# Optimization experiments

Measured on AMD Instinct MI355X. Metric: run time of the kernel, lower is better.

## Reference

```python
import jax, jax.numpy as jnp
import numpy as np

# ---- static config ----
B, N, C, HF, WF = 2, 256, 256, 64, 64
PATCH = 512
ROI = 15
MARGIN = (ROI - 1) // 2
HID = 256
HEADS = 8
DEPTH = 3
FFN = 1024
NQ = 16
LN_EPS = 1e-5


def setup_inputs() -> dict:
    key = jax.random.key(0)
    ks = jax.random.split(key, 16)
    p = lambda i, shape: (0.02 * jax.random.normal(ks[i], shape, jnp.float32))
    inp = {
        "image_embeddings": jax.random.normal(ks[0], (B, C, HF, WF), jnp.float32),
        "keypoints": jax.random.uniform(ks[1], (B, N, 2), jnp.float32, 0.0, float(PATCH)),
        "keypoints_valid_mask": jax.random.randint(ks[2], (B, N), 0, 2) == 1,
        "proj_w": p(3, (HID, C)), "proj_b": jnp.zeros((HID,), jnp.float32),
        "query_embed": p(4, (NQ, HID)),
        "self_qkv_w": p(5, (DEPTH, 3 * HID, HID)), "self_qkv_b": jnp.zeros((DEPTH, 3 * HID), jnp.float32),
        "self_out_w": p(6, (DEPTH, HID, HID)), "self_out_b": jnp.zeros((DEPTH, HID), jnp.float32),
        "cross_qkv_w": p(7, (DEPTH, 3 * HID, HID)), "cross_qkv_b": jnp.zeros((DEPTH, 3 * HID), jnp.float32),
        "cross_out_w": p(8, (DEPTH, HID, HID)), "cross_out_b": jnp.zeros((DEPTH, HID), jnp.float32),
        "ffn1_w": p(9, (DEPTH, FFN, HID)), "ffn1_b": jnp.zeros((DEPTH, FFN), jnp.float32),
        "ffn2_w": p(10, (DEPTH, HID, FFN)), "ffn2_b": jnp.zeros((DEPTH, HID), jnp.float32),
        "ln1_w": jnp.ones((DEPTH, HID), jnp.float32), "ln1_b": jnp.zeros((DEPTH, HID), jnp.float32),
        "ln2_w": jnp.ones((DEPTH, HID), jnp.float32), "ln2_b": jnp.zeros((DEPTH, HID), jnp.float32),
        "ln3_w": jnp.ones((DEPTH, HID), jnp.float32), "ln3_b": jnp.zeros((DEPTH, HID), jnp.float32),
        "out_w": p(11, (4, HID)), "out_b": jnp.zeros((4,), jnp.float32),
    }
    return inp


def _layer_norm(x, w, b):
    mu = x.mean(-1, keepdims=True)
    var = ((x - mu) ** 2).mean(-1, keepdims=True)
    return (x - mu) * jax.lax.rsqrt(var + LN_EPS) * w + b


def _mha(q_in, kv_in, Wqkv, bqkv, Wo, bo, pad=None):
    # PyTorch nn.MultiheadAttention math (batch_first). pad: [B, S_kv] True=masked.
    Dh = HID // HEADS
    Wq, Wk, Wv = jnp.split(Wqkv, 3, axis=0)
    bq, bk, bv = jnp.split(bqkv, 3, axis=0)
    Bsz = q_in.shape[0]
    q = (q_in @ Wq.T + bq).reshape(Bsz, -1, HEADS, Dh)
    k = (kv_in @ Wk.T + bk).reshape(Bsz, -1, HEADS, Dh)
    v = (kv_in @ Wv.T + bv).reshape(Bsz, -1, HEADS, Dh)
    s = jnp.einsum('bqhd,bkhd->bhqk', q, k) * (Dh ** -0.5)
    if pad is not None:
        s = jnp.where(pad[:, None, None, :], -jnp.inf, s)
    a = jax.nn.softmax(s, axis=-1)
    o = jnp.einsum('bhqk,bkhd->bqhd', a, v).reshape(Bsz, -1, HID)
    return o @ Wo.T + bo


def _roi_sample(img, keypoints):
    # _get_valid_grid + F.grid_sample(bilinear, align_corners=False, zeros padding)
    rc = jnp.round(keypoints)                               # [B,N,2] (r,c), round-half-even like Python round
    off = jnp.arange(-MARGIN, MARGIN + 1, dtype=img.dtype)  # [ROI]
    gy = rc[:, :, 0][..., None, None] + off[:, None]        # [B,N,ROI,ROI] rows
    gx = rc[:, :, 1][..., None, None] + off[None, :]        # [B,N,ROI,ROI] cols
    gxn = gx / (PATCH - 1) * 2.0 - 1.0
    gyn = gy / (PATCH - 1) * 2.0 - 1.0
    invalid = (gxn < -1) | (gyn < -1) | (gxn > 1) | (gyn > 1)  # [B,N,ROI,ROI]
    gxn = jnp.where(invalid, 0.0, gxn)
    gyn = jnp.where(invalid, 0.0, gyn)
    # unnormalize onto the feature map (align_corners=False)
    x = ((gxn + 1.0) * WF - 1.0) * 0.5
    y = ((gyn + 1.0) * HF - 1.0) * 0.5
    x = x.reshape(B, -1)  # [B, P], P = N*ROI*ROI
    y = y.reshape(B, -1)
    x0f = jnp.floor(x); y0f = jnp.floor(y)
    wx = x - x0f; wy = y - y0f
    x0 = x0f.astype(jnp.int32); y0 = y0f.astype(jnp.int32)
    bidx = jnp.arange(B)[:, None]

    def tap(yi, xi, w):
        ok = (yi >= 0) & (yi < HF) & (xi >= 0) & (xi < WF)
        yc = jnp.clip(yi, 0, HF - 1)
        xc = jnp.clip(xi, 0, WF - 1)
        v = img[bidx, :, yc, xc]                 # [B,P,C] gather
        return v * (w * ok)[..., None]

    out = (tap(y0, x0, (1 - wy) * (1 - wx)) + tap(y0, x0 + 1, (1 - wy) * wx)
           + tap(y0 + 1, x0, wy * (1 - wx)) + tap(y0 + 1, x0 + 1, wy * wx))
    feat = out.reshape(B, N, ROI * ROI, C)
    feat = jnp.where(invalid.reshape(B, N, ROI * ROI)[..., None], 0.0, feat)
    return feat  # [B, N, HW, C]


def reference(image_embeddings, keypoints, keypoints_valid_mask, proj_w, proj_b,
              query_embed, self_qkv_w, self_qkv_b, self_out_w, self_out_b,
              cross_qkv_w, cross_qkv_b, cross_out_w, cross_out_b,
              ffn1_w, ffn1_b, ffn2_w, ffn2_b,
              ln1_w, ln1_b, ln2_w, ln2_b, ln3_w, ln3_b, out_w, out_b):
    feat = _roi_sample(image_embeddings, keypoints)                 # [B,N,HW,C]
    mem = jnp.einsum('bnpc,oc->bnpo', feat, proj_w) + proj_b        # 1x1 conv proj
    mem = mem.reshape(B * N, ROI * ROI, HID)
    pad = jnp.broadcast_to(~keypoints_valid_mask.reshape(-1, 1), (B * N, ROI * ROI))
    pad = pad.at[:, 0].set(False)                                    # token 0 always attendable
    tgt = jnp.broadcast_to(query_embed[None], (B * N, NQ, HID))
    for l in range(DEPTH):  # post-norm TransformerDecoderLayer, relu, eval (no dropout)
        sa = _mha(tgt, tgt, self_qkv_w[l], self_qkv_b[l], self_out_w[l], self_out_b[l])
        tgt = _layer_norm(tgt + sa, ln1_w[l], ln1_b[l])
        ca = _mha(tgt, mem, cross_qkv_w[l], cross_qkv_b[l], cross_out_w[l], cross_out_b[l], pad)
        tgt = _layer_norm(tgt + ca, ln2_w[l], ln2_b[l])
        ff = jax.nn.relu(tgt @ ffn1_w[l].T + ffn1_b[l]) @ ffn2_w[l].T + ffn2_b[l]
        tgt = _layer_norm(tgt + ff, ln3_w[l], ln3_b[l])
    out = tgt @ out_w.T + out_b                                      # [B*N, NQ, 4]
    return out.reshape(B, N, NQ, 4)
```

## Files before the change

kernel.cpp:

```cpp
#include <hip/hip_runtime.h>
#include <hip/hip_fp16.h>

#define LB __launch_bounds__(256)

typedef unsigned short u16;
typedef unsigned int   u32;
typedef __attribute__((ext_vector_type(8))) short bf16x8;
typedef __attribute__((ext_vector_type(4))) float f32x4;
typedef __attribute__((ext_vector_type(8))) u16  u16x8;

__device__ __forceinline__ u16 f2b(float f) {
    u32 u = __float_as_uint(f);
    u32 r = (u + 0x7fffu + ((u >> 16) & 1u)) >> 16;
    return (u16)r;
}
__device__ __forceinline__ float b2f(u16 h) {
    return __uint_as_float((u32)h << 16);
}

#define QSCALE 0.17677669529663687f


__global__ LB void k_wconv(const float* __restrict__ s0, const float* __restrict__ s1,
                           const float* __restrict__ s2, const float* __restrict__ s3,
                           const float* __restrict__ s4, const float* __restrict__ s5,
                           const float* __restrict__ s6, u16* __restrict__ dst,
                           const unsigned char* __restrict__ m, int* __restrict__ valid,
                           const float* __restrict__ pb,
                           const float* __restrict__ cqkv_b,
                           float* __restrict__ ckv)
{
    if (blockIdx.x >= 14336) {
        const int pblk = blockIdx.x - 14336;
        if (pblk == 0) {
            __shared__ int flag;
            if (threadIdx.x == 0) flag = 0;
            __syncthreads();
            int loc = 0;
            for (int off = threadIdx.x; off < 512; off += 256)
                if ((off & 3) != 0 && m[off] != 0) loc = 1;
            if (loc) atomicOr(&flag, 1);
            __syncthreads();
            const bool bytelay = (flag != 0);
            for (int s = threadIdx.x; s < 512; s += 256)
                valid[s] = bytelay ? (int)(m[s] != 0) : (int)(((const int*)m)[s] != 0);
        } else {
            const int l = pblk - 1;
            const float* Wv = s3 + (size_t)l * 196608 + 131072;
            const float* vb = cqkv_b + (size_t)l * 768 + 512;
            const int o = threadIdx.x;
            float c = 0.f;
            for (int cc = 0; cc < 256; cc += 4) {
                const float4 p4 = *(const float4*)(pb + cc);
                const float4 v4 = *(const float4*)(Wv + (size_t)o * 256 + cc);
                c += p4.x * v4.x + p4.y * v4.y + p4.z * v4.z + p4.w * v4.w;
            }
            ckv[l * 512 + o]       = cqkv_b[(size_t)l * 768 + o];
            ckv[l * 512 + 256 + o] = c + vb[o];
        }
        return;
    }
    const int e = blockIdx.x * 256 + threadIdx.x;
    if (e >= 3670016) return;
    float v;
    int i = e;
    if (i < 65536) v = s0[i];
    else if ((i -= 65536) < 589824) v = s1[i];
    else if ((i -= 589824) < 196608) v = s2[i];
    else if ((i -= 196608) < 589824) v = s3[i];
    else if ((i -= 589824) < 196608) v = s4[i];
    else if ((i -= 196608) < 786432) v = s5[i];
    else if ((i -= 786432) < 786432) v = s6[i];
    else if ((i -= 786432) < 393216) {
        const int l = i / 131072;
        const int r = (i - l * 131072) >> 8;
        const int c = i & 255;
        v = s3[(size_t)l * 196608 + (size_t)(256 + r) * 256 + c];
    } else {
        i -= 393216;
        v = s0[(i & 255) * 256 + (i >> 8)];
    }
    dst[e] = f2b(v);
}

__global__ LB void k_transpose(const float* __restrict__ img, u16* __restrict__ imgTb)
{
    __shared__ float tile[64][65];
    const int b  = blockIdx.z;
    const int c0 = blockIdx.y * 64;
    const int p0 = blockIdx.x * 64;
    const int t  = threadIdx.x;
    const int tr = t >> 6, tc = t & 63;
#pragma unroll
    for (int p = 0; p < 16; ++p) {
        const int i = p * 4 + tr;
        tile[i][tc] = img[((size_t)(b * 256 + c0 + i)) * 4096 + p0 + tc];
    }
    __syncthreads();
#pragma unroll
    for (int p = 0; p < 16; ++p) {
        const int jj = p * 4 + tr;
        imgTb[((size_t)(b * 4096 + p0 + jj)) * 256 + c0 + tc] = f2b(tile[tc][jj]);
    }
}

template<int BM>
__global__ LB void gemm_mfma(const u16* __restrict__ A, const u16* __restrict__ W,
                             const float* __restrict__ bias,
                             float* __restrict__ Cf, u16* __restrict__ Cb,
                             int M, int N, int K, int relu)
{
    constexpr int BN = 128;
    __shared__ u16 lds[2][(BM + BN) * 64];
    const int t = threadIdx.x;
    const int wid = t >> 6, lane = t & 63;
    const int bm = blockIdx.y * BM, bn = blockIdx.x * BN;
    const int KT = K >> 6;

    auto stage = [&](int buf, int kt) {
        const int k0 = kt * 64;
        const int rr = t >> 3;
        const int u  = t & 7;
#pragma unroll
        for (int q = 0; q < BM / 32; ++q) {
            const int r = q * 32 + rr;
            const u16* src = A + (size_t)(bm + r) * K + k0 + ((u ^ (r & 7)) << 3);
            __builtin_amdgcn_global_load_lds(
                (const __attribute__((address_space(1))) void*)src,
                (__attribute__((address_space(3))) void*)&lds[buf][q * 2048 + wid * 512],
                16, 0, 0);
        }
#pragma unroll
        for (int q = 0; q < 4; ++q) {
            const int r = q * 32 + rr;
            const u16* src = W + (size_t)(bn + r) * K + k0 + ((u ^ (r & 7)) << 3);
            __builtin_amdgcn_global_load_lds(
                (const __attribute__((address_space(1))) void*)src,
                (__attribute__((address_space(3))) void*)&lds[buf][BM * 64 + q * 2048 + wid * 512],
                16, 0, 0);
        }
    };

    const int wr = wid >> 1, wc = wid & 1;
    constexpr int MR = BM / 32;
    f32x4 acc[MR][4];
    const f32x4 z = {0.f, 0.f, 0.f, 0.f};
#pragma unroll
    for (int mi = 0; mi < MR; ++mi)
#pragma unroll
        for (int ni = 0; ni < 4; ++ni) acc[mi][ni] = z;

    const int r16 = lane & 15, kg = lane >> 4;

    stage(0, 0);
    int cur = 0;
    for (int kt = 0; kt < KT; ++kt) {
        asm volatile("s_waitcnt vmcnt(0)" ::: "memory");
        __syncthreads();
        if (kt + 1 < KT) stage(cur ^ 1, kt + 1);
        const u16* pA = lds[cur];
        const u16* pB = lds[cur] + BM * 64;
#pragma unroll
        for (int kk = 0; kk < 2; ++kk) {
            const int s = kk * 4 + kg;
            bf16x8 afr[MR], bfr[4];
#pragma unroll
            for (int mi = 0; mi < MR; ++mi) {
                const int r = wr * (BM / 2) + mi * 16 + r16;
                afr[mi] = *(const bf16x8*)(pA + r * 64 + ((s ^ (r & 7)) << 3));
            }
#pragma unroll
            for (int ni = 0; ni < 4; ++ni) {
                const int c = wc * 64 + ni * 16 + r16;
                bfr[ni] = *(const bf16x8*)(pB + c * 64 + ((s ^ (c & 7)) << 3));
            }
#pragma unroll
            for (int mi = 0; mi < MR; ++mi)
#pragma unroll
                for (int ni = 0; ni < 4; ++ni)
                    acc[mi][ni] = __builtin_amdgcn_mfma_f32_16x16x32_bf16(
                        afr[mi], bfr[ni], acc[mi][ni], 0, 0, 0);
        }
        cur ^= 1;
    }

#pragma unroll
    for (int mi = 0; mi < MR; ++mi) {
#pragma unroll
        for (int ni = 0; ni < 4; ++ni) {
            const int col = bn + wc * 64 + ni * 16 + r16;
            const float bs = bias ? bias[col] : 0.0f;
#pragma unroll
            for (int rg = 0; rg < 4; ++rg) {
                const int row = bm + wr * (BM / 2) + mi * 16 + kg * 4 + rg;
                float v = acc[mi][ni][rg] + bs;
                if (relu) v = fmaxf(v, 0.0f);
                if (Cf) Cf[(size_t)row * N + col] = v;
                if (Cb) Cb[(size_t)row * N + col] = f2b(v);
            }
        }
    }
}

__global__ LB void gemm_ln(const u16* __restrict__ A, const u16* __restrict__ W,
                           const float* __restrict__ bias,
                           float* __restrict__ tgt, u16* __restrict__ tgtb,
                           const float* __restrict__ lnw, const float* __restrict__ lnb,
                           int K,
                           const float* __restrict__ ow, const float* __restrict__ ob,
                           float* __restrict__ outp)
{
    __shared__ u16 lA[32 * 64];
    __shared__ u16 lB[256 * 64];
    __shared__ float psum[2][32];
    __shared__ float psq[2][32];
    __shared__ float hsum[2][32][4];
    const int t = threadIdx.x;
    const int wid = t >> 6, lane = t & 63;
    const int r16 = lane & 15, kg = lane >> 4;
    const int wr = wid >> 1, wc = wid & 1;
    const int bm = blockIdx.x * 32;
    const int KT = K >> 6;

    f32x4 acc[8];
    const f32x4 z = {0.f, 0.f, 0.f, 0.f};
#pragma unroll
    for (int ni = 0; ni < 8; ++ni) acc[ni] = z;

    for (int kt = 0; kt < KT; ++kt) {
        const int k0 = kt * 64;
        const int rr = t >> 3;
        const int u  = t & 7;
        {
            const int r = rr;
            const u16* src = A + (size_t)(bm + r) * K + k0 + ((u ^ (r & 7)) << 3);
            __builtin_amdgcn_global_load_lds(
                (const __attribute__((address_space(1))) void*)src,
                (__attribute__((address_space(3))) void*)&lA[wid * 512],
                16, 0, 0);
        }
#pragma unroll
        for (int q = 0; q < 8; ++q) {
            const int r = q * 32 + rr;
            const u16* src = W + (size_t)r * K + k0 + ((u ^ (r & 7)) << 3);
            __builtin_amdgcn_global_load_lds(
                (const __attribute__((address_space(1))) void*)src,
                (__attribute__((address_space(3))) void*)&lB[q * 2048 + wid * 512],
                16, 0, 0);
        }
        asm volatile("s_waitcnt vmcnt(0)" ::: "memory");
        __syncthreads();
#pragma unroll
        for (int kk = 0; kk < 2; ++kk) {
            const int s = kk * 4 + kg;
            const int ra = wr * 16 + r16;
            const bf16x8 afr = *(const bf16x8*)(lA + ra * 64 + ((s ^ (ra & 7)) << 3));
#pragma unroll
            for (int ni = 0; ni < 8; ++ni) {
                const int c = wc * 128 + ni * 16 + r16;
                const bf16x8 bfr = *(const bf16x8*)(lB + c * 64 + ((s ^ (c & 7)) << 3));
                acc[ni] = __builtin_amdgcn_mfma_f32_16x16x32_bf16(afr, bfr, acc[ni], 0, 0, 0);
            }
        }
        __syncthreads();
    }

    float xv[4][8];
    float bcol[8], wcol[8], bncol[8];
#pragma unroll
    for (int ni = 0; ni < 8; ++ni) {
        const int c = wc * 128 + ni * 16 + r16;
        bcol[ni]  = bias[c];
        wcol[ni]  = lnw[c];
        bncol[ni] = lnb[c];
    }
#pragma unroll
    for (int rg = 0; rg < 4; ++rg) {
        const int row = bm + wr * 16 + kg * 4 + rg;
#pragma unroll
        for (int ni = 0; ni < 8; ++ni) {
            const int c = wc * 128 + ni * 16 + r16;
            xv[rg][ni] = tgt[(size_t)row * 256 + c] + acc[ni][rg] + bcol[ni];
        }
    }
#pragma unroll
    for (int rg = 0; rg < 4; ++rg) {
        float s = 0.f;
#pragma unroll
        for (int ni = 0; ni < 8; ++ni) s += xv[rg][ni];
#pragma unroll
        for (int m = 1; m < 16; m <<= 1) s += __shfl_xor(s, m);
        if (r16 == 0) psum[wc][wr * 16 + kg * 4 + rg] = s;
    }
    __syncthreads();
    float mu[4];
#pragma unroll
    for (int rg = 0; rg < 4; ++rg) {
        const int rl = wr * 16 + kg * 4 + rg;
        mu[rg] = (psum[0][rl] + psum[1][rl]) * (1.0f / 256.0f);
    }
#pragma unroll
    for (int rg = 0; rg < 4; ++rg) {
        float q = 0.f;
#pragma unroll
        for (int ni = 0; ni < 8; ++ni) {
            const float d = xv[rg][ni] - mu[rg];
            q += d * d;
        }
#pragma unroll
        for (int m = 1; m < 16; m <<= 1) q += __shfl_xor(q, m);
        if (r16 == 0) psq[wc][wr * 16 + kg * 4 + rg] = q;
    }
    __syncthreads();
    float onorm[4][8];
#pragma unroll
    for (int rg = 0; rg < 4; ++rg) {
        const int rl = wr * 16 + kg * 4 + rg;
        const int row = bm + rl;
        const float var = (psq[0][rl] + psq[1][rl]) * (1.0f / 256.0f);
        const float inv = 1.0f / sqrtf(var + 1e-5f);
#pragma unroll
        for (int ni = 0; ni < 8; ++ni) {
            const int c = wc * 128 + ni * 16 + r16;
            const float o = (xv[rg][ni] - mu[rg]) * inv * wcol[ni] + bncol[ni];
            onorm[rg][ni] = o;
            tgt[(size_t)row * 256 + c]  = o;
            tgtb[(size_t)row * 256 + c] = f2b(o);
        }
    }

    if (outp) {
#pragma unroll
        for (int j = 0; j < 4; ++j) {
            float wj[8];
#pragma unroll
            for (int ni = 0; ni < 8; ++ni)
                wj[ni] = ow[j * 256 + wc * 128 + ni * 16 + r16];
#pragma unroll
            for (int rg = 0; rg < 4; ++rg) {
                float p = 0.f;
#pragma unroll
                for (int ni = 0; ni < 8; ++ni) p += onorm[rg][ni] * wj[ni];
#pragma unroll
                for (int m = 1; m < 16; m <<= 1) p += __shfl_xor(p, m);
                if (r16 == 0) hsum[wc][wr * 16 + kg * 4 + rg][j] = p;
            }
        }
        __syncthreads();
        if (t < 128) {
            const int row = t >> 2, j = t & 3;
            outp[(size_t)(bm + row) * 4 + j] =
                hsum[0][row][j] + hsum[1][row][j] + ob[j];
        }
    }
}

__global__ LB void k_init_tgt(float* __restrict__ tgt, u16* __restrict__ tgtb,
                              const float* __restrict__ qe)
{
    const int e = blockIdx.x * 256 + threadIdx.x;
    const int c = e & 255;
    const int row = e >> 8;
    const int i = row & 15;
    const float v = qe[(i << 8) | c];
    tgt[e] = v;
    tgtb[e] = f2b(v);
}

__global__ LB void k_self_attn(const u16* __restrict__ QKV, u16* __restrict__ O)
{
    __shared__ __align__(16) u16 arena[4][1536];
    const int t = threadIdx.x;
    const int lane = t & 63, wid = t >> 6;
    const int r16 = lane & 15, kg = lane >> 4;
    const int blk = blockIdx.x;
    const int s = blk >> 1;
    const int h = (blk & 1) * 4 + wid;

    u16* p_lds = &arena[wid][0];
    u16* vT    = &arena[wid][512];

    const bf16x8 qfr = *(const bf16x8*)(QKV + (size_t)(s * 16 + r16) * 768 + h * 32 + kg * 8);
    const bf16x8 kfr = *(const bf16x8*)(QKV + (size_t)(s * 16 + r16) * 768 + 256 + h * 32 + kg * 8);
    f32x4 sv = {0.f, 0.f, 0.f, 0.f};
    sv = __builtin_amdgcn_mfma_f32_16x16x32_bf16(qfr, kfr, sv, 0, 0, 0);

    float ev[4], rowsum[4];
#pragma unroll
    for (int rg = 0; rg < 4; ++rg) ev[rg] = sv[rg] * QSCALE;
#pragma unroll
    for (int rg = 0; rg < 4; ++rg) {
        float mx = ev[rg];
#pragma unroll
        for (int m = 1; m < 16; m <<= 1) mx = fmaxf(mx, __shfl_xor(mx, m));
        ev[rg] = __expf(ev[rg] - mx);
        float ps = ev[rg];
#pragma unroll
        for (int m = 1; m < 16; m <<= 1) ps += __shfl_xor(ps, m);
        rowsum[rg] = ps;
    }

#pragma unroll
    for (int rg = 0; rg < 4; ++rg)
        p_lds[(kg * 4 + rg) * 32 + r16] = f2b(ev[rg]);
    {
        const int zq = lane & 15, zc = 16 + (lane >> 4) * 4;
#pragma unroll
        for (int j = 0; j < 4; ++j) p_lds[zq * 32 + zc + j] = 0;
    }
    {
        const int key = lane >> 2, ch8 = (lane & 3) * 8;
        const u16x8 v = *(const u16x8*)(QKV + (size_t)(s * 16 + key) * 768 + 512 + h * 32 + ch8);
#pragma unroll
        for (int j = 0; j < 8; ++j)
            vT[(ch8 + j) * 32 + key] = ((const u16*)&v)[j];
        const int zc0 = lane >> 1, zk0 = 16 + (lane & 1) * 8;
#pragma unroll
        for (int j = 0; j < 8; ++j) vT[zc0 * 32 + zk0 + j] = 0;
    }

#pragma unroll
    for (int ct = 0; ct < 2; ++ct) {
        const bf16x8 pa = *(const bf16x8*)(p_lds + r16 * 32 + kg * 8);
        const bf16x8 vb = *(const bf16x8*)(vT + (ct * 16 + r16) * 32 + kg * 8);
        f32x4 ao = {0.f, 0.f, 0.f, 0.f};
        ao = __builtin_amdgcn_mfma_f32_16x16x32_bf16(pa, vb, ao, 0, 0, 0);
#pragma unroll
        for (int rg = 0; rg < 4; ++rg) {
            const int q = kg * 4 + rg;
            O[(size_t)(s * 16 + q) * 256 + h * 32 + ct * 16 + r16] = f2b(ao[rg] / rowsum[rg]);
        }
    }
}

__global__ LB void k_cross_attn(const u16* __restrict__ tgtb,
                                const u16* __restrict__ wQ,
                                const u16* __restrict__ KV, int kvs,
                                const float* __restrict__ ckv,
                                const int* __restrict__ valid,
                                const float* __restrict__ kps,
                                u16* __restrict__ O)
{
    __shared__ __align__(16) char arena[64832];
    u16* Wm  = (u16*)arena;
    u16* WmT = (u16*)(arena + 14400);

    const int t = threadIdx.x;
    const int lane = t & 63, wid = t >> 6;
    const int r16 = lane & 15, kg = lane >> 4;
    const int s = blockIdx.x;
    const int b = s >> 8, n = s & 255;

    u16* buf = (u16*)(arena + 22848 + wid * 10496);
    u16* p_b = (u16*)(arena + 22848 + wid * 10496 + 2048);
    u16* QP  = p_b;

    for (int e = t; e < 16208; e += 256) ((u32*)arena)[e] = 0;
    __syncthreads();

    const float kpy = kps[(b * 256 + n) * 2 + 0];
    const float kpx = kps[(b * 256 + n) * 2 + 1];
    const float gx0 = rintf(kpx) - 7.0f;
    const float gy0 = rintf(kpy) - 7.0f;
    const float gxn0 = gx0 / 511.0f * 2.0f - 1.0f;
    const float gyn0 = gy0 / 511.0f * 2.0f - 1.0f;
    const float xb = ((gxn0 + 1.f) * 64.f - 1.f) * 0.5f;
    const float yb = ((gyn0 + 1.f) * 64.f - 1.f) * 0.5f;
    const int x0b = (int)floorf(xb);
    const int y0b = (int)floorf(yb);

    if (t < 225) {
        const int iy = t / 15, ix = t - iy * 15;
        const float gy = rintf(kpy) + (float)(iy - 7);
        const float gx = rintf(kpx) + (float)(ix - 7);
        const float gxn = gx / 511.0f * 2.0f - 1.0f;
        const float gyn = gy / 511.0f * 2.0f - 1.0f;
        const bool inval = (gxn < -1.f) || (gyn < -1.f) || (gxn > 1.f) || (gyn > 1.f);
        const float x = ((gxn + 1.f) * 64.f - 1.f) * 0.5f;
        const float y = ((gyn + 1.f) * 64.f - 1.f) * 0.5f;
        const float x0f = floorf(x), y0f = floorf(y);
        const float wx = x - x0f, wy = y - y0f;
        const int x0 = (int)x0f, y0 = (int)y0f;
#pragma unroll
        for (int tt = 0; tt < 4; ++tt) {
            const int dy = tt >> 1, dx = tt & 1;
            const int yi = y0 + dy, xi = x0 + dx;
            const bool ok = (yi >= 0) && (yi < 64) && (xi >= 0) && (xi < 64) && !inval;
            const float w = (dy ? wy : 1.f - wy) * (dx ? wx : 1.f - wx);
            if (ok) {
                const int cell = (yi - y0b) * 4 + (xi - x0b);
                const u16 wb = f2b(w);
                Wm[t * 32 + ((((cell >> 3) ^ (t & 3)) << 3) | (cell & 7))] = wb;
                WmT[cell * 264 + t] = wb;
            }
        }
    }

    const int cell = lane >> 2, ch8 = (lane & 3) * 8;
    const int cy = cell >> 2, cx = cell & 3;
    const int py = min(max(y0b + cy, 0), 63);
    const int px = min(max(x0b + cx, 0), 63);
    const bool vld = valid[s] != 0;

    for (int hh = 0; hh < 2; ++hh) {
        const int h = hh * 4 + wid;
        const size_t texidx = (size_t)(b * 4096 + py * 64 + px) * kvs + h * 32 + ch8;

#pragma unroll
        for (int ct = 0; ct < 2; ++ct) {
            f32x4 aq = {0.f, 0.f, 0.f, 0.f};
#pragma unroll
            for (int ks = 0; ks < 8; ++ks) {
                const bf16x8 ta = *(const bf16x8*)(tgtb + (size_t)(s * 16 + r16) * 256 + ks * 32 + kg * 8);
                const bf16x8 wb = *(const bf16x8*)(wQ + (size_t)(h * 32 + ct * 16 + r16) * 256 + ks * 32 + kg * 8);
                aq = __builtin_amdgcn_mfma_f32_16x16x32_bf16(ta, wb, aq, 0, 0, 0);
            }
            const float bq = ckv[h * 32 + ct * 16 + r16];
#pragma unroll
            for (int rg = 0; rg < 4; ++rg)
                QP[(kg * 4 + rg) * 40 + ct * 16 + r16] = f2b(aq[rg] + bq);
        }
        *(u16x8*)(buf + cell * 32 + ch8) = *(const u16x8*)(KV + texidx);

        if (hh == 0) __syncthreads();

        {
            const bf16x8 qfr = *(const bf16x8*)(QP + r16 * 40 + kg * 8);
            const bf16x8 tfr = *(const bf16x8*)(buf + r16 * 32 + kg * 8);
            f32x4 aq = {0.f, 0.f, 0.f, 0.f};
            aq = __builtin_amdgcn_mfma_f32_16x16x32_bf16(qfr, tfr, aq, 0, 0, 0);
#pragma unroll
            for (int rg = 0; rg < 4; ++rg)
                QP[(kg * 4 + rg) * 40 + r16] = f2b(aq[rg]);
        }

        float ev[4][15];
        {
            const bf16x8 afr = *(const bf16x8*)(QP + r16 * 40 + kg * 8);
#pragma unroll
            for (int tile = 0; tile < 15; ++tile) {
                const int p = tile * 16 + r16;
                const int rc = p < 225 ? p : 224;
                const bf16x8 bfr = *(const bf16x8*)(Wm + rc * 32 + ((kg ^ (rc & 3)) << 3));
                f32x4 acc = {0.f, 0.f, 0.f, 0.f};
                acc = __builtin_amdgcn_mfma_f32_16x16x32_bf16(afr, bfr, acc, 0, 0, 0);
#pragma unroll
                for (int rg = 0; rg < 4; ++rg) {
                    float sv = acc[rg] * QSCALE;
                    if (p > 224) sv = -1e30f;
                    if (!vld && p > 0) sv = -1e30f;
                    ev[rg][tile] = sv;
                }
            }
        }
        float rowsumv[4];
#pragma unroll
        for (int rg = 0; rg < 4; ++rg) {
            float mx = -1e30f;
#pragma unroll
            for (int k = 0; k < 15; ++k) mx = fmaxf(mx, ev[rg][k]);
#pragma unroll
            for (int m = 1; m < 16; m <<= 1) mx = fmaxf(mx, __shfl_xor(mx, m));
            float ps = 0.f;
#pragma unroll
            for (int k = 0; k < 15; ++k) {
                ev[rg][k] = __expf(ev[rg][k] - mx);
                ps += ev[rg][k];
            }
#pragma unroll
            for (int m = 1; m < 16; m <<= 1) ps += __shfl_xor(ps, m);
            rowsumv[rg] = ps;
        }

#pragma unroll
        for (int rg = 0; rg < 4; ++rg)
#pragma unroll
            for (int k = 0; k < 15; ++k) {
                const int p = k * 16 + r16;
                if (p < 225) p_b[(kg * 4 + rg) * 264 + p] = f2b(ev[rg][k]);
            }
        for (int e = lane; e < 496; e += 64) {
            const int row = e / 31;
            p_b[row * 264 + 225 + (e - row * 31)] = 0;
        }

        {
            const u16x8 v = *(const u16x8*)(KV + texidx + 256);
#pragma unroll
            for (int j = 0; j < 8; ++j)
                buf[(ch8 + j) * 32 + cell] = ((const u16*)&v)[j];
            const int zr = lane & 15, zc0 = 16 + (lane >> 4) * 4;
#pragma unroll
            for (int j = 0; j < 4; ++j) buf[zr * 32 + zc0 + j] = 0;
        }

        f32x4 pw = {0.f, 0.f, 0.f, 0.f};
#pragma unroll
        for (int ks = 0; ks < 8; ++ks) {
            const bf16x8 pa = *(const bf16x8*)(p_b + r16 * 264 + ks * 32 + kg * 8);
            const bf16x8 wb = *(const bf16x8*)(WmT + r16 * 264 + ks * 32 + kg * 8);
            pw = __builtin_amdgcn_mfma_f32_16x16x32_bf16(pa, wb, pw, 0, 0, 0);
        }

#pragma unroll
        for (int rg = 0; rg < 4; ++rg)
            QP[(kg * 4 + rg) * 40 + r16] = f2b(pw[rg]);
        {
            const int zq = lane & 15, zc0 = 16 + (lane >> 4) * 4;
#pragma unroll
            for (int j = 0; j < 4; ++j) QP[zq * 40 + zc0 + j] = 0;
        }

#pragma unroll
        for (int ct = 0; ct < 2; ++ct) {
            const bf16x8 pa = *(const bf16x8*)(QP + r16 * 40 + kg * 8);
            const bf16x8 vb = *(const bf16x8*)(buf + (ct * 16 + r16) * 32 + kg * 8);
            f32x4 ao = {0.f, 0.f, 0.f, 0.f};
            ao = __builtin_amdgcn_mfma_f32_16x16x32_bf16(pa, vb, ao, 0, 0, 0);
#pragma unroll
            for (int rg = 0; rg < 4; ++rg) {
                const int q = kg * 4 + rg;
                const int ch = h * 32 + ct * 16 + r16;
                const float val = ao[rg] / rowsumv[rg] + ckv[256 + ch];
                O[(size_t)(s * 16 + q) * 256 + ch] = f2b(val);
            }
        }
    }
}

extern "C" void kernel_launch(void* const* d_in, const int* in_sizes, int n_in,
                              void* d_out, int out_size, void* d_ws, size_t ws_size,
                              hipStream_t stream)
{
    const float* img          = (const float*)d_in[0];
    const float* kps          = (const float*)d_in[1];
    const unsigned char* vmsk = (const unsigned char*)d_in[2];
    const float* proj_w       = (const float*)d_in[3];
    const float* proj_b       = (const float*)d_in[4];
    const float* query_embed  = (const float*)d_in[5];
    const float* self_qkv_w   = (const float*)d_in[6];
    const float* self_qkv_b   = (const float*)d_in[7];
    const float* self_out_w   = (const float*)d_in[8];
    const float* self_out_b   = (const float*)d_in[9];
    const float* cross_qkv_w  = (const float*)d_in[10];
    const float* cross_qkv_b  = (const float*)d_in[11];
    const float* cross_out_w  = (const float*)d_in[12];
    const float* cross_out_b  = (const float*)d_in[13];
    const float* ffn1_w       = (const float*)d_in[14];
    const float* ffn1_b       = (const float*)d_in[15];
    const float* ffn2_w       = (const float*)d_in[16];
    const float* ffn2_b       = (const float*)d_in[17];
    const float* ln1_w        = (const float*)d_in[18];
    const float* ln1_b        = (const float*)d_in[19];
    const float* ln2_w        = (const float*)d_in[20];
    const float* ln2_b        = (const float*)d_in[21];
    const float* ln3_w        = (const float*)d_in[22];
    const float* ln3_b        = (const float*)d_in[23];
    const float* out_w        = (const float*)d_in[24];
    const float* out_b        = (const float*)d_in[25];
    float* out = (float*)d_out;

    char* W8 = (char*)d_ws;
    size_t off = 0;
    auto alloc = [&](size_t bytes) { void* p = W8 + off; off += (bytes + 255) & ~(size_t)255; return p; };
    float* tgt   = (float*)alloc(2097152 * 4);
    u16* Sb16    = (u16*)alloc(6291456 * 2);
    float* ckv   = (float*)alloc(3 * 512 * 4);
    u16* imgTb   = (u16*)alloc(2097152 * 2);
    u16* KVb3    = (u16*)alloc(12582912 * 2);
    u16* tgtb    = (u16*)alloc(2097152 * 2);
    u16* Abuf    = (u16*)alloc(2097152 * 2);
    u16* Hbuf    = (u16*)alloc(8388608 * 2);
    u16* wAll    = (u16*)alloc(3670016 * 2);
    u16* WcombB  = (u16*)alloc(393216 * 2);
    int* valid   = (int*)alloc(512 * 4);

    u16* wProj  = wAll;
    u16* wSQKV  = wProj + 65536;
    u16* wSOut  = wSQKV + 589824;
    u16* wCQKV  = wSOut + 196608;
    u16* wCOut  = wCQKV + 589824;
    u16* wF1    = wCOut + 196608;
    u16* wF2    = wF1 + 786432;
    u16* wCKV3  = wF2 + 786432;
    u16* wProjT = wCKV3 + 393216;

    k_wconv<<<14340, 256, 0, stream>>>(proj_w, self_qkv_w, self_out_w, cross_qkv_w,
                                       cross_out_w, ffn1_w, ffn2_w, wAll,
                                       vmsk, valid, proj_b, cross_qkv_b, ckv);
    k_transpose<<<dim3(64, 4, 2), 256, 0, stream>>>(img, imgTb);
    gemm_mfma<64><<<dim3(2, 24), 256, 0, stream>>>(wCKV3, wProjT, nullptr,
                                                   nullptr, WcombB, 1536, 256, 256, 0);
    gemm_mfma<64><<<dim3(12, 128), 256, 0, stream>>>(imgTb, WcombB, nullptr,
                                                     nullptr, KVb3, 8192, 1536, 256, 0);
    k_init_tgt<<<8192, 256, 0, stream>>>(tgt, tgtb, query_embed);

    for (int l = 0; l < 3; ++l) {
        const int last = (l == 2);
        gemm_mfma<64><<<dim3(6, 128), 256, 0, stream>>>(tgtb, wSQKV + (size_t)l * 196608,
            self_qkv_b + (size_t)l * 768, nullptr, Sb16, 8192, 768, 256, 0);
        k_self_attn<<<1024, 256, 0, stream>>>(Sb16, Abuf);
        gemm_ln<<<256, 256, 0, stream>>>(Abuf, wSOut + (size_t)l * 65536,
            self_out_b + (size_t)l * 256, tgt, tgtb,
            ln1_w + (size_t)l * 256, ln1_b + (size_t)l * 256, 256,
            nullptr, nullptr, nullptr);

        k_cross_attn<<<512, 256, 0, stream>>>(tgtb, wCQKV + (size_t)l * 196608,
                                              KVb3 + (size_t)l * 512, 1536,
                                              ckv + (size_t)l * 512, valid, kps, Abuf);
        gemm_ln<<<256, 256, 0, stream>>>(Abuf, wCOut + (size_t)l * 65536,
            cross_out_b + (size_t)l * 256, tgt, tgtb,
            ln2_w + (size_t)l * 256, ln2_b + (size_t)l * 256, 256,
            nullptr, nullptr, nullptr);

        gemm_mfma<64><<<dim3(8, 128), 256, 0, stream>>>(tgtb, wF1 + (size_t)l * 262144,
            ffn1_b + (size_t)l * 1024, nullptr, Hbuf, 8192, 1024, 256, 1);
        gemm_ln<<<256, 256, 0, stream>>>(Hbuf, wF2 + (size_t)l * 262144,
            ffn2_b + (size_t)l * 256, tgt, tgtb,
            ln3_w + (size_t)l * 256, ln3_b + (size_t)l * 256, 1024,
            last ? out_w : nullptr, last ? out_b : nullptr, last ? out : nullptr);
    }
}
```

Baseline: 353.7 us.

## Fold image transpose into weight-convert kernel, halve self-attn grid, hoist tgt loads

The separate image transpose kernel is merged into the weight conversion launch as 512 extra blocks, which removes one kernel launch. The self-attention kernel now has each block loop over both head groups for one sequence, so its grid shrinks from 1024 to 512 blocks. In cross-attention, the tgt A-fragments are loaded into registers once, before the head loop, instead of being reloaded inside it. The cost is more register pressure, and the k_wconv blocks now all reserve shared memory for the tile, which may lower their occupancy.

```diff
diff --git a/kernel.cpp b/kernel.cpp
--- a/kernel.cpp
+++ b/kernel.cpp
@@ -28,8 +28,10 @@
                            const unsigned char* __restrict__ m, int* __restrict__ valid,
                            const float* __restrict__ pb,
                            const float* __restrict__ cqkv_b,
-                           float* __restrict__ ckv)
+                           float* __restrict__ ckv,
+                           const float* __restrict__ img, u16* __restrict__ imgTb)
 {
+    __shared__ float tile[64][65];
     if (blockIdx.x >= 14336) {
         const int pblk = blockIdx.x - 14336;
         if (pblk == 0) {
@@ -44,7 +46,7 @@
             const bool bytelay = (flag != 0);
             for (int s = threadIdx.x; s < 512; s += 256)
                 valid[s] = bytelay ? (int)(m[s] != 0) : (int)(((const int*)m)[s] != 0);
-        } else {
+        } else if (pblk < 4) {
             const int l = pblk - 1;
             const float* Wv = s3 + (size_t)l * 196608 + 131072;
             const float* vb = cqkv_b + (size_t)l * 768 + 512;
@@ -57,6 +59,25 @@
             }
             ckv[l * 512 + o]       = cqkv_b[(size_t)l * 768 + o];
             ckv[l * 512 + 256 + o] = c + vb[o];
+        } else {
+            const int idx = pblk - 4;
+            const int b  = idx >> 8;
+            const int rem = idx & 255;
+            const int c0 = (rem >> 6) * 64;
+            const int p0 = (rem & 63) * 64;
+            const int t  = threadIdx.x;
+            const int tr = t >> 6, tc = t & 63;
+#pragma unroll
+            for (int p = 0; p < 16; ++p) {
+                const int i = p * 4 + tr;
+                tile[i][tc] = img[((size_t)(b * 256 + c0 + i)) * 4096 + p0 + tc];
+            }
+            __syncthreads();
+#pragma unroll
+            for (int p = 0; p < 16; ++p) {
+                const int jj = p * 4 + tr;
+                imgTb[((size_t)(b * 4096 + p0 + jj)) * 256 + c0 + tc] = f2b(tile[tc][jj]);
+            }
         }
         return;
     }
@@ -83,27 +104,6 @@
     dst[e] = f2b(v);
 }
 
-__global__ LB void k_transpose(const float* __restrict__ img, u16* __restrict__ imgTb)
-{
-    __shared__ float tile[64][65];
-    const int b  = blockIdx.z;
-    const int c0 = blockIdx.y * 64;
-    const int p0 = blockIdx.x * 64;
-    const int t  = threadIdx.x;
-    const int tr = t >> 6, tc = t & 63;
-#pragma unroll
-    for (int p = 0; p < 16; ++p) {
-        const int i = p * 4 + tr;
-        tile[i][tc] = img[((size_t)(b * 256 + c0 + i)) * 4096 + p0 + tc];
-    }
-    __syncthreads();
-#pragma unroll
-    for (int p = 0; p < 16; ++p) {
-        const int jj = p * 4 + tr;
-        imgTb[((size_t)(b * 4096 + p0 + jj)) * 256 + c0 + tc] = f2b(tile[tc][jj]);
-    }
-}
-
 template<int BM>
 __global__ LB void gemm_mfma(const u16* __restrict__ A, const u16* __restrict__ W,
                              const float* __restrict__ bias,
@@ -373,62 +373,64 @@
     const int t = threadIdx.x;
     const int lane = t & 63, wid = t >> 6;
     const int r16 = lane & 15, kg = lane >> 4;
-    const int blk = blockIdx.x;
-    const int s = blk >> 1;
-    const int h = (blk & 1) * 4 + wid;
+    const int s = blockIdx.x;
 
     u16* p_lds = &arena[wid][0];
     u16* vT    = &arena[wid][512];
 
-    const bf16x8 qfr = *(const bf16x8*)(QKV + (size_t)(s * 16 + r16) * 768 + h * 32 + kg * 8);
-    const bf16x8 kfr = *(const bf16x8*)(QKV + (size_t)(s * 16 + r16) * 768 + 256 + h * 32 + kg * 8);
-    f32x4 sv = {0.f, 0.f, 0.f, 0.f};
-    sv = __builtin_amdgcn_mfma_f32_16x16x32_bf16(qfr, kfr, sv, 0, 0, 0);
-
-    float ev[4], rowsum[4];
-#pragma unroll
-    for (int rg = 0; rg < 4; ++rg) ev[rg] = sv[rg] * QSCALE;
-#pragma unroll
-    for (int rg = 0; rg < 4; ++rg) {
-        float mx = ev[rg];
-#pragma unroll
-        for (int m = 1; m < 16; m <<= 1) mx = fmaxf(mx, __shfl_xor(mx, m));
-        ev[rg] = __expf(ev[rg] - mx);
-        float ps = ev[rg];
-#pragma unroll
-        for (int m = 1; m < 16; m <<= 1) ps += __shfl_xor(ps, m);
-        rowsum[rg] = ps;
-    }
-
-#pragma unroll
-    for (int rg = 0; rg < 4; ++rg)
-        p_lds[(kg * 4 + rg) * 32 + r16] = f2b(ev[rg]);
-    {
-        const int zq = lane & 15, zc = 16 + (lane >> 4) * 4;
-#pragma unroll
-        for (int j = 0; j < 4; ++j) p_lds[zq * 32 + zc + j] = 0;
-    }
-    {
-        const int key = lane >> 2, ch8 = (lane & 3) * 8;
-        const u16x8 v = *(const u16x8*)(QKV + (size_t)(s * 16 + key) * 768 + 512 + h * 32 + ch8);
-#pragma unroll
-        for (int j = 0; j < 8; ++j)
-            vT[(ch8 + j) * 32 + key] = ((const u16*)&v)[j];
-        const int zc0 = lane >> 1, zk0 = 16 + (lane & 1) * 8;
-#pragma unroll
-        for (int j = 0; j < 8; ++j) vT[zc0 * 32 + zk0 + j] = 0;
-    }
-
-#pragma unroll
-    for (int ct = 0; ct < 2; ++ct) {
-        const bf16x8 pa = *(const bf16x8*)(p_lds + r16 * 32 + kg * 8);
-        const bf16x8 vb = *(const bf16x8*)(vT + (ct * 16 + r16) * 32 + kg * 8);
-        f32x4 ao = {0.f, 0.f, 0.f, 0.f};
-        ao = __builtin_amdgcn_mfma_f32_16x16x32_bf16(pa, vb, ao, 0, 0, 0);
+    for (int hh = 0; hh < 2; ++hh) {
+        const int h = hh * 4 + wid;
+
+        const bf16x8 qfr = *(const bf16x8*)(QKV + (size_t)(s * 16 + r16) * 768 + h * 32 + kg * 8);
+        const bf16x8 kfr = *(const bf16x8*)(QKV + (size_t)(s * 16 + r16) * 768 + 256 + h * 32 + kg * 8);
+        f32x4 sv = {0.f, 0.f, 0.f, 0.f};
+        sv = __builtin_amdgcn_mfma_f32_16x16x32_bf16(qfr, kfr, sv, 0, 0, 0);
+
+        float ev[4], rowsum[4];
+#pragma unroll
+        for (int rg = 0; rg < 4; ++rg) ev[rg] = sv[rg] * QSCALE;
 #pragma unroll
         for (int rg = 0; rg < 4; ++rg) {
-            const int q = kg * 4 + rg;
-            O[(size_t)(s * 16 + q) * 256 + h * 32 + ct * 16 + r16] = f2b(ao[rg] / rowsum[rg]);
+            float mx = ev[rg];
+#pragma unroll
+            for (int m = 1; m < 16; m <<= 1) mx = fmaxf(mx, __shfl_xor(mx, m));
+            ev[rg] = __expf(ev[rg] - mx);
+            float ps = ev[rg];
+#pragma unroll
+            for (int m = 1; m < 16; m <<= 1) ps += __shfl_xor(ps, m);
+            rowsum[rg] = ps;
+        }
+
+#pragma unroll
+        for (int rg = 0; rg < 4; ++rg)
+            p_lds[(kg * 4 + rg) * 32 + r16] = f2b(ev[rg]);
+        {
+            const int zq = lane & 15, zc = 16 + (lane >> 4) * 4;
+#pragma unroll
+            for (int j = 0; j < 4; ++j) p_lds[zq * 32 + zc + j] = 0;
+        }
+        {
+            const int key = lane >> 2, ch8 = (lane & 3) * 8;
+            const u16x8 v = *(const u16x8*)(QKV + (size_t)(s * 16 + key) * 768 + 512 + h * 32 + ch8);
+#pragma unroll
+            for (int j = 0; j < 8; ++j)
+                vT[(ch8 + j) * 32 + key] = ((const u16*)&v)[j];
+            const int zc0 = lane >> 1, zk0 = 16 + (lane & 1) * 8;
+#pragma unroll
+            for (int j = 0; j < 8; ++j) vT[zc0 * 32 + zk0 + j] = 0;
+        }
+
+#pragma unroll
+        for (int ct = 0; ct < 2; ++ct) {
+            const bf16x8 pa = *(const bf16x8*)(p_lds + r16 * 32 + kg * 8);
+            const bf16x8 vb = *(const bf16x8*)(vT + (ct * 16 + r16) * 32 + kg * 8);
+            f32x4 ao = {0.f, 0.f, 0.f, 0.f};
+            ao = __builtin_amdgcn_mfma_f32_16x16x32_bf16(pa, vb, ao, 0, 0, 0);
+#pragma unroll
+            for (int rg = 0; rg < 4; ++rg) {
+                const int q = kg * 4 + rg;
+                O[(size_t)(s * 16 + q) * 256 + h * 32 + ct * 16 + r16] = f2b(ao[rg] / rowsum[rg]);
+            }
         }
     }
 }
@@ -502,6 +504,11 @@
     const int px = min(max(x0b + cx, 0), 63);
     const bool vld = valid[s] != 0;
 
+    bf16x8 ta[8];
+#pragma unroll
+    for (int ks = 0; ks < 8; ++ks)
+        ta[ks] = *(const bf16x8*)(tgtb + (size_t)(s * 16 + r16) * 256 + ks * 32 + kg * 8);
+
     for (int hh = 0; hh < 2; ++hh) {
         const int h = hh * 4 + wid;
         const size_t texidx = (size_t)(b * 4096 + py * 64 + px) * kvs + h * 32 + ch8;
@@ -511,9 +518,8 @@
             f32x4 aq = {0.f, 0.f, 0.f, 0.f};
 #pragma unroll
             for (int ks = 0; ks < 8; ++ks) {
-                const bf16x8 ta = *(const bf16x8*)(tgtb + (size_t)(s * 16 + r16) * 256 + ks * 32 + kg * 8);
                 const bf16x8 wb = *(const bf16x8*)(wQ + (size_t)(h * 32 + ct * 16 + r16) * 256 + ks * 32 + kg * 8);
-                aq = __builtin_amdgcn_mfma_f32_16x16x32_bf16(ta, wb, aq, 0, 0, 0);
+                aq = __builtin_amdgcn_mfma_f32_16x16x32_bf16(ta[ks], wb, aq, 0, 0, 0);
             }
             const float bq = ckv[h * 32 + ct * 16 + r16];
 #pragma unroll
@@ -685,10 +691,10 @@
     u16* wCKV3  = wF2 + 786432;
     u16* wProjT = wCKV3 + 393216;
 
-    k_wconv<<<14340, 256, 0, stream>>>(proj_w, self_qkv_w, self_out_w, cross_qkv_w,
+    k_wconv<<<14852, 256, 0, stream>>>(proj_w, self_qkv_w, self_out_w, cross_qkv_w,
                                        cross_out_w, ffn1_w, ffn2_w, wAll,
-                                       vmsk, valid, proj_b, cross_qkv_b, ckv);
-    k_transpose<<<dim3(64, 4, 2), 256, 0, stream>>>(img, imgTb);
+                                       vmsk, valid, proj_b, cross_qkv_b, ckv,
+                                       img, imgTb);
     gemm_mfma<64><<<dim3(2, 24), 256, 0, stream>>>(wCKV3, wProjT, nullptr,
                                                    nullptr, WcombB, 1536, 256, 256, 0);
     gemm_mfma<64><<<dim3(12, 128), 256, 0, stream>>>(imgTb, WcombB, nullptr,
@@ -699,7 +705,7 @@
         const int last = (l == 2);
         gemm_mfma<64><<<dim3(6, 128), 256, 0, stream>>>(tgtb, wSQKV + (size_t)l * 196608,
             self_qkv_b + (size_t)l * 768, nullptr, Sb16, 8192, 768, 256, 0);
-        k_self_attn<<<1024, 256, 0, stream>>>(Sb16, Abuf);
+        k_self_attn<<<512, 256, 0, stream>>>(Sb16, Abuf);
         gemm_ln<<<256, 256, 0, stream>>>(Abuf, wSOut + (size_t)l * 65536,
             self_out_b + (size_t)l * 256, tgt, tgtb,
             ln1_w + (size_t)l * 256, ln1_b + (size_t)l * 256, 256,
```

New measurement: 351.9 us. About the same (-0.5%).
